# Kernel optimization log

Measured on AMD Instinct MI355X. Metric: run time of the kernel, lower is better.

## Reference

```python
import jax, jax.numpy as jnp
import numpy as np

N, E, H, F_IN, F_OUT = 100000, 1600000, 4, 128, 32
SLOPE = 0.2


def setup_inputs() -> dict:
    key = jax.random.key(0)
    ks = jax.random.split(key, 5)
    x = jax.random.normal(ks[0], (N, F_IN), dtype=jnp.float32)
    edge_src = jax.random.randint(ks[1], (E,), 0, N)
    edge_dst = jax.random.randint(ks[2], (E,), 0, N)
    # xavier-ish init (gain 1.414) as in reset_parameters
    weight = jax.random.normal(ks[3], (H, F_IN, F_OUT), dtype=jnp.float32) * (1.414 / np.sqrt(F_IN))
    a = jax.random.normal(ks[4], (H, 2 * F_OUT), dtype=jnp.float32) * (1.414 / np.sqrt(2 * F_OUT))
    bias = jnp.zeros((H, F_OUT), dtype=jnp.float32)
    return {"x": x, "weight": weight, "a": a, "bias": bias,
            "edge_src": edge_src, "edge_dst": edge_dst}


def reference(x, weight, a, bias, edge_src, edge_dst):
    # per-head linear transform: [N,H,F_OUT]
    h = jnp.einsum('nf,hfo->nho', x, weight)
    # split attention vector: e_ij = LeakyReLU(a_src.h_i + a_dst.h_j)
    a_src, a_dst = a[:, :F_OUT], a[:, F_OUT:]
    alpha_src = jnp.einsum('nho,ho->nh', h, a_src)  # [N,H]
    alpha_dst = jnp.einsum('nho,ho->nh', h, a_dst)  # [N,H]
    e = jax.nn.leaky_relu(alpha_src[edge_src] + alpha_dst[edge_dst], SLOPE)  # [E,H]
    # numerically-stable edge softmax over incoming edges of each dst node
    e_max = jax.ops.segment_max(e, edge_dst, num_segments=N)  # [N,H]
    e_max = jnp.where(jnp.isfinite(e_max), e_max, 0.0)        # nodes with no in-edges
    e_exp = jnp.exp(e - e_max[edge_dst])                      # [E,H]
    denom = jax.ops.segment_sum(e_exp, edge_dst, num_segments=N)  # [N,H]
    att = e_exp / (denom[edge_dst] + 1e-16)                   # [E,H]
    # weighted aggregation: out[j] = sum_i att_ij * h_i
    msg = h[edge_src] * att[:, :, None]                       # [E,H,F_OUT]
    out = jax.ops.segment_sum(msg, edge_dst, num_segments=N)  # [N,H,F_OUT]
    out = out + bias                                          # broadcast [H,F_OUT]
    return out.reshape(N, H * F_OUT)                          # multi-head concat
```

## Files before the change

kernel.cpp:

```cpp
#include <hip/hip_runtime.h>

#define NN   100000
#define NE   1600000
#define NH   4
#define FIN  128
#define FOUT 32
#define HF   128
#define SLOPE 0.2f

#define PBKT  64
#define PNB   ((NN+PBKT-1)/PBKT)
#define CAP   2048
#define EPB   16384
#define NEB   ((NE+EPB-1)/EPB)
#define LCSR  768

typedef __attribute__((ext_vector_type(8))) short short8v;
typedef __attribute__((ext_vector_type(4))) float f32x4;

__device__ __forceinline__ unsigned int bpack(float lo, float hi){
    unsigned int ul = __float_as_uint(lo), uh = __float_as_uint(hi);
    ul = (ul + 0x7fffu + ((ul>>16)&1u)) >> 16;
    uh = (uh + 0x7fffu + ((uh>>16)&1u)) >> 16;
    return ul | (uh<<16);
}
__device__ __forceinline__ short bf16of(float f){
    unsigned int u = __float_as_uint(f);
    return (short)((u + 0x7fffu + ((u>>16)&1u)) >> 16);
}

__global__ __launch_bounds__(256) void node_mfma(
    const float* __restrict__ x, const float* __restrict__ w,
    const float* __restrict__ wa, unsigned int* __restrict__ hb,
    float* __restrict__ asrc, float* __restrict__ adst)
{
    __shared__ short xs[64*128];
    char* lds = (char*)xs;
    const int t  = threadIdx.x;
    const int n0 = blockIdx.x*64;

    #pragma unroll
    for (int p=0; p<8; ++p){
        int r  = p*8 + (t>>5);
        int cq = t & 31;
        int nr = n0 + r; if (nr > NN-1) nr = NN-1;
        float4 v = *(const float4*)(x + (size_t)nr*FIN + cq*4);
        unsigned int lo = bpack(v.x, v.y), hi = bpack(v.z, v.w);
        int cb = (cq*8) ^ ((r&7)<<4);
        *(uint2*)(lds + r*256 + cb) = make_uint2(lo, hi);
    }
    __syncthreads();

    const int wv   = t>>6;
    const int lane = t&63;
    const int l15  = lane&15;
    const int lk   = (lane>>4)<<3;

    short8v Bf[3][4];
    #pragma unroll
    for (int cf=0; cf<2; ++cf){
        int col = wv*32 + cf*16 + l15;
        const float* wp = w + (size_t)(col>>5)*4096 + (col&31);
        #pragma unroll
        for (int ks=0; ks<4; ++ks){
            short8v b;
            #pragma unroll
            for (int j=0;j<8;j++)
                b[j] = bf16of(wp[(size_t)(ks*32 + lk + j)*32]);
            Bf[cf][ks] = b;
        }
    }
    if (wv==0){
        const float* wap = wa + l15*128;
        #pragma unroll
        for (int ks=0; ks<4; ++ks){
            short8v b;
            #pragma unroll
            for (int j=0;j<8;j++){
                float v = (l15<8) ? wap[ks*32 + lk + j] : 0.f;
                b[j] = bf16of(v);
            }
            Bf[2][ks] = b;
        }
    }

    f32x4 C[4][3];
    #pragma unroll
    for (int rt=0;rt<4;rt++)
        #pragma unroll
        for (int cf=0;cf<3;cf++){ f32x4 z = {0.f,0.f,0.f,0.f}; C[rt][cf] = z; }

    const int axor = (lane&7)<<4;
    #pragma unroll
    for (int rt=0; rt<4; ++rt){
        int row = rt*16 + l15;
        const char* arow = lds + row*256;
        short8v Af[4];
        #pragma unroll
        for (int ks=0; ks<4; ++ks)
            Af[ks] = *(const short8v*)(arow + (((ks<<6) | (lk<<1)) ^ axor));
        #pragma unroll
        for (int ks=0; ks<4; ++ks){
            C[rt][0] = __builtin_amdgcn_mfma_f32_16x16x32_bf16(Af[ks], Bf[0][ks], C[rt][0], 0,0,0);
            C[rt][1] = __builtin_amdgcn_mfma_f32_16x16x32_bf16(Af[ks], Bf[1][ks], C[rt][1], 0,0,0);
            if (wv==0)
                C[rt][2] = __builtin_amdgcn_mfma_f32_16x16x32_bf16(Af[ks], Bf[2][ks], C[rt][2], 0,0,0);
        }
    }

    const int g4 = l15>>2;
    #pragma unroll
    for (int rt=0; rt<4; ++rt){
        #pragma unroll
        for (int cf=0; cf<2; ++cf){
            f32x4 c = C[rt][cf];
            #pragma unroll
            for (int i=0;i<4;i++){
                float v1 = __shfl_xor(c[i], 1);
                float v2 = __shfl_xor(c[i], 2);
                float v3 = __shfl_xor(c[i], 3);
                int node = n0 + rt*16 + ((lane>>4)<<2) + i;
                if ((l15&3)==0 && node < NN){
                    uint2 pk = make_uint2(bpack(c[i], v1), bpack(v2, v3));
                    *(uint2*)(hb + (size_t)node*64 + wv*16 + cf*8 + g4*2) = pk;
                }
            }
        }
    }
    if (wv==0 && l15 < 8){
        #pragma unroll
        for (int rt=0; rt<4; ++rt){
            f32x4 c = C[rt][2];
            #pragma unroll
            for (int i=0;i<4;i++){
                int node = n0 + rt*16 + ((lane>>4)<<2) + i;
                if (node < NN){
                    if (l15 < 4) asrc[(size_t)node*4 + l15]     = c[i];
                    else         adst[(size_t)node*4 + (l15-4)] = c[i];
                }
            }
        }
    }
}

__global__ __launch_bounds__(1024) void part_k(const int* __restrict__ esrc,
                                               const int* __restrict__ edst,
                                               int* __restrict__ cnt,
                                               unsigned int* __restrict__ parr,
                                               const float* __restrict__ w,
                                               const float* __restrict__ a,
                                               float* __restrict__ wa)
{
    int t = threadIdx.x;
    if (blockIdx.x == 0){
        int s = t>>7, f = t&127, h = s&3;
        const float* ap = a + h*64 + (s>>2)*32;
        const float* wp = w + (size_t)h*4096 + f*32;
        float acc = 0.f;
        #pragma unroll
        for (int o=0;o<32;o++) acc = fmaf(wp[o], ap[o], acc);
        wa[s*128 + f] = acc;
    }
    __shared__ int hist[PNB];
    __shared__ int bcur[PNB];
    for (int i=t;i<PNB;i+=1024) hist[i]=0;
    __syncthreads();
    int base = blockIdx.x*EPB;
    #pragma unroll
    for (int k=0;k<16;k++){
        int e = base + k*1024 + t;
        if (e < NE) atomicAdd(&hist[edst[e]>>6], 1);
    }
    __syncthreads();
    for (int i=t;i<PNB;i+=1024)
        bcur[i] = hist[i] ? atomicAdd(&cnt[i], hist[i]) : 0;
    __syncthreads();
    #pragma unroll
    for (int k=0;k<16;k++){
        int e = base + k*1024 + t;
        if (e < NE){
            int d = edst[e], s = esrc[e];
            int b = d>>6;
            int pos = atomicAdd(&bcur[b], 1);
            parr[(size_t)b*CAP + pos] = ((unsigned int)s<<6) | (unsigned int)(d & 63);
        }
    }
}

__global__ __launch_bounds__(256) void gather_k(
    const int* __restrict__ cnt,
    const unsigned int* __restrict__ parr,
    const float* __restrict__ asrc, const float* __restrict__ adst,
    const unsigned int* __restrict__ hb, const float* __restrict__ bias,
    float* __restrict__ out)
{
    __shared__ int lcount[32], loffs[32], lcur[32];
    __shared__ int lcsr[LCSR];
    int b = blockIdx.x, bkt = b>>1, half = b&1;
    int t = threadIdx.x;
    int cb = cnt[bkt];
    const unsigned int* pb = parr + (size_t)bkt*CAP;

    if (t < 32) lcount[t] = 0;
    __syncthreads();
    for (int i=t;i<cb;i+=256){
        unsigned int dl = pb[i] & 63u;
        if ((int)(dl>>5) == half) atomicAdd(&lcount[dl&31], 1);
    }
    __syncthreads();
    if (t < 32){
        int v = lcount[t];
        int x = v;
        #pragma unroll
        for (int off=1; off<32; off<<=1){
            int y = __shfl_up(x, off);
            if (t >= off) x += y;
        }
        loffs[t] = x - v;
        lcur[t]  = x - v;
    }
    __syncthreads();
    for (int i=t;i<cb;i+=256){
        unsigned int en = pb[i];
        unsigned int dl = en & 63u;
        if ((int)(dl>>5) == half){
            int pos = atomicAdd(&lcur[dl&31], 1);
            if (pos < LCSR) lcsr[pos] = (int)(en >> 6);
        }
    }
    __syncthreads();

    int wv = t>>6, lane = t&63, head = lane>>4;
    float2 bi = *(const float2*)(bias + 2*lane);
    const unsigned int* hoff = hb + lane;
    int dbase = bkt*PBKT + half*32;

    for (int dl = wv; dl < 32; dl += 4){
        int d = dbase + dl;
        if (d >= NN) break;
        int st = loffs[dl];
        int en = st + lcount[dl];
        if (st > LCSR) st = LCSR;
        if (en > LCSR) en = LCSR;

        float ad_h = adst[(size_t)d*NH + head];
        float ssum = 0.f, acc0 = 0.f, acc1 = 0.f;

        int i = st;
        for (; i + 8 <= en; i += 8){
            int s[8]; float av[8]; unsigned int u[8];
            #pragma unroll
            for (int k=0;k<8;k++) s[k] = lcsr[i+k];
            #pragma unroll
            for (int k=0;k<8;k++) av[k] = asrc[(size_t)s[k]*NH + head];
            #pragma unroll
            for (int k=0;k<8;k++) u[k] = hoff[(size_t)s[k]*64];
            #pragma unroll
            for (int k=0;k<8;k++){
                float v = av[k] + ad_h;
                v = v > 0.f ? v : SLOPE*v;
                float p = __expf(v);
                ssum += p;
                acc0 = fmaf(p, __uint_as_float(u[k]<<16),        acc0);
                acc1 = fmaf(p, __uint_as_float(u[k]&0xffff0000u), acc1);
            }
        }
        for (; i < en; ++i){
            int s = lcsr[i];
            float av = asrc[(size_t)s*NH + head];
            unsigned int u = hoff[(size_t)s*64];
            float v = av + ad_h;
            v = v > 0.f ? v : SLOPE*v;
            float p = __expf(v);
            ssum += p;
            acc0 = fmaf(p, __uint_as_float(u<<16),        acc0);
            acc1 = fmaf(p, __uint_as_float(u&0xffff0000u), acc1);
        }
        float inv = 1.f / (ssum + 1e-16f);
        float2 o = make_float2(acc0*inv + bi.x, acc1*inv + bi.y);
        *(float2*)(out + (size_t)d*HF + 2*lane) = o;
    }
}

extern "C" void kernel_launch(void* const* d_in, const int* in_sizes, int n_in,
                              void* d_out, int out_size, void* d_ws, size_t ws_size,
                              hipStream_t stream)
{
    const float* x    = (const float*)d_in[0];
    const float* w    = (const float*)d_in[1];
    const float* a    = (const float*)d_in[2];
    const float* bias = (const float*)d_in[3];
    const int* esrc   = (const int*)d_in[4];
    const int* edst   = (const int*)d_in[5];
    float* out = (float*)d_out;

    unsigned int* hb = (unsigned int*)d_ws;
    float* as   = (float*)(hb + (size_t)NN*64);
    float* ad   = as + (size_t)NN*NH;
    int* cnt    = (int*)(ad + (size_t)NN*NH);
    unsigned int* parr = (unsigned int*)(cnt + PNB);
    float* wa   = (float*)(parr + (size_t)PNB*CAP);

    hipMemsetAsync(cnt, 0, PNB*sizeof(int), stream);
    hipLaunchKernelGGL(part_k, dim3(NEB), dim3(1024), 0, stream,
                       esrc, edst, cnt, parr, w, a, wa);
    hipLaunchKernelGGL(node_mfma, dim3((NN+63)/64), dim3(256), 0, stream,
                       x, w, wa, hb, as, ad);
    hipLaunchKernelGGL(gather_k, dim3(PNB*2), dim3(256), 0, stream,
                       cnt, parr, as, ad, hb, bias, out);
}
```

Before: 151.8 us.

## Precompute bf16 weight fragments, replace memset, interleave two dst nodes in gather

Adds a single-block prep kernel that folds the attention vector into the weights, packs the weight and attention-weight MFMA B fragments into bf16 once, and zeroes the bucket counters in place of the memset. node_mfma then loads ready-made fragments instead of every block doing strided fp32 loads and conversions. gather_k now has each wave process two destination nodes together in chunks of 4 edges, so more independent gathers are in flight to hide latency. The cost is an extra serial launch before part_k and somewhat higher register use in gather.

```diff
diff --git a/kernel.cpp b/kernel.cpp
--- a/kernel.cpp
+++ b/kernel.cpp
@@ -28,10 +28,50 @@
     unsigned int u = __float_as_uint(f);
     return (short)((u + 0x7fffu + ((u>>16)&1u)) >> 16);
 }
+__device__ __forceinline__ float blo(unsigned int u){ return __uint_as_float(u<<16); }
+__device__ __forceinline__ float bhi(unsigned int u){ return __uint_as_float(u&0xffff0000u); }
+
+__global__ __launch_bounds__(1024) void prep_k(
+    const float* __restrict__ w, const float* __restrict__ a,
+    short* __restrict__ wfrag, short* __restrict__ wafrag,
+    int* __restrict__ cnt)
+{
+    __shared__ float wal[1024];
+    int t = threadIdx.x;
+    {
+        int s = t>>7, f = t&127, h = s&3;
+        const float* ap = a + h*64 + (s>>2)*32;
+        const float* wp = w + (size_t)h*4096 + f*32;
+        float acc = 0.f;
+        #pragma unroll
+        for (int o=0;o<32;o++) acc = fmaf(wp[o], ap[o], acc);
+        wal[s*128 + f] = acc;
+    }
+    __syncthreads();
+    for (int idx=t; idx<2048; idx+=1024){
+        int lane = idx&63, ks=(idx>>6)&3, cf=(idx>>8)&1, wvv=idx>>9;
+        int col = wvv*32 + cf*16 + (lane&15);
+        int fb  = ks*32 + (lane>>4)*8;
+        const float* wp = w + (size_t)(col>>5)*4096 + (col&31);
+        short8v bv;
+        #pragma unroll
+        for (int j=0;j<8;j++) bv[j] = bf16of(wp[(size_t)(fb+j)*32]);
+        ((short8v*)wfrag)[idx] = bv;
+    }
+    if (t < 256){
+        int lane = t&63, ks = t>>6;
+        int l15 = lane&15, fb = ks*32 + (lane>>4)*8;
+        short8v bv;
+        #pragma unroll
+        for (int j=0;j<8;j++) bv[j] = (l15<8) ? bf16of(wal[l15*128 + fb + j]) : (short)0;
+        ((short8v*)wafrag)[t] = bv;
+    }
+    for (int i=t;i<PNB;i+=1024) cnt[i]=0;
+}
 
 __global__ __launch_bounds__(256) void node_mfma(
-    const float* __restrict__ x, const float* __restrict__ w,
-    const float* __restrict__ wa, unsigned int* __restrict__ hb,
+    const float* __restrict__ x, const short* __restrict__ wfrag,
+    const short* __restrict__ wafrag, unsigned int* __restrict__ hb,
     float* __restrict__ asrc, float* __restrict__ adst)
 {
     __shared__ short xs[64*128];
@@ -57,31 +97,16 @@
     const int lk   = (lane>>4)<<3;
 
     short8v Bf[3][4];
-    #pragma unroll
-    for (int cf=0; cf<2; ++cf){
-        int col = wv*32 + cf*16 + l15;
-        const float* wp = w + (size_t)(col>>5)*4096 + (col&31);
-        #pragma unroll
-        for (int ks=0; ks<4; ++ks){
-            short8v b;
-            #pragma unroll
-            for (int j=0;j<8;j++)
-                b[j] = bf16of(wp[(size_t)(ks*32 + lk + j)*32]);
-            Bf[cf][ks] = b;
-        }
-    }
+    const short8v* wf  = (const short8v*)wfrag;
+    const short8v* waf = (const short8v*)wafrag;
+    #pragma unroll
+    for (int cf=0; cf<2; ++cf)
+        #pragma unroll
+        for (int ks=0; ks<4; ++ks)
+            Bf[cf][ks] = wf[((wv*2+cf)*4+ks)*64 + lane];
     if (wv==0){
-        const float* wap = wa + l15*128;
-        #pragma unroll
-        for (int ks=0; ks<4; ++ks){
-            short8v b;
-            #pragma unroll
-            for (int j=0;j<8;j++){
-                float v = (l15<8) ? wap[ks*32 + lk + j] : 0.f;
-                b[j] = bf16of(v);
-            }
-            Bf[2][ks] = b;
-        }
+        #pragma unroll
+        for (int ks=0; ks<4; ++ks) Bf[2][ks] = waf[ks*64 + lane];
     }
 
     f32x4 C[4][3];
@@ -146,23 +171,11 @@
 __global__ __launch_bounds__(1024) void part_k(const int* __restrict__ esrc,
                                                const int* __restrict__ edst,
                                                int* __restrict__ cnt,
-                                               unsigned int* __restrict__ parr,
-                                               const float* __restrict__ w,
-                                               const float* __restrict__ a,
-                                               float* __restrict__ wa)
-{
-    int t = threadIdx.x;
-    if (blockIdx.x == 0){
-        int s = t>>7, f = t&127, h = s&3;
-        const float* ap = a + h*64 + (s>>2)*32;
-        const float* wp = w + (size_t)h*4096 + f*32;
-        float acc = 0.f;
-        #pragma unroll
-        for (int o=0;o<32;o++) acc = fmaf(wp[o], ap[o], acc);
-        wa[s*128 + f] = acc;
-    }
+                                               unsigned int* __restrict__ parr)
+{
     __shared__ int hist[PNB];
     __shared__ int bcur[PNB];
+    int t = threadIdx.x;
     for (int i=t;i<PNB;i+=1024) hist[i]=0;
     __syncthreads();
     int base = blockIdx.x*EPB;
@@ -187,6 +200,39 @@
     }
 }
 
+__device__ __forceinline__ void edge4(const int* __restrict__ lcsr, int i, int head,
+    float ad_h, const float* __restrict__ asrc, const unsigned int* __restrict__ hoff,
+    float& ssum, float& acc0, float& acc1)
+{
+    int s0=lcsr[i], s1=lcsr[i+1], s2=lcsr[i+2], s3=lcsr[i+3];
+    float a0=asrc[(size_t)s0*NH+head], a1=asrc[(size_t)s1*NH+head];
+    float a2=asrc[(size_t)s2*NH+head], a3=asrc[(size_t)s3*NH+head];
+    unsigned int u0=hoff[(size_t)s0*64], u1=hoff[(size_t)s1*64];
+    unsigned int u2=hoff[(size_t)s2*64], u3=hoff[(size_t)s3*64];
+    float v0=a0+ad_h; v0 = v0>0.f ? v0 : SLOPE*v0;
+    float v1=a1+ad_h; v1 = v1>0.f ? v1 : SLOPE*v1;
+    float v2=a2+ad_h; v2 = v2>0.f ? v2 : SLOPE*v2;
+    float v3=a3+ad_h; v3 = v3>0.f ? v3 : SLOPE*v3;
+    float p0=__expf(v0), p1=__expf(v1), p2=__expf(v2), p3=__expf(v3);
+    ssum += (p0+p1)+(p2+p3);
+    acc0 = fmaf(p0,blo(u0), fmaf(p1,blo(u1), fmaf(p2,blo(u2), fmaf(p3,blo(u3), acc0))));
+    acc1 = fmaf(p0,bhi(u0), fmaf(p1,bhi(u1), fmaf(p2,bhi(u2), fmaf(p3,bhi(u3), acc1))));
+}
+__device__ __forceinline__ void edge1(const int* __restrict__ lcsr, int i, int head,
+    float ad_h, const float* __restrict__ asrc, const unsigned int* __restrict__ hoff,
+    float& ssum, float& acc0, float& acc1)
+{
+    int s = lcsr[i];
+    float av = asrc[(size_t)s*NH+head];
+    unsigned int u = hoff[(size_t)s*64];
+    float v = av + ad_h;
+    v = v > 0.f ? v : SLOPE*v;
+    float p = __expf(v);
+    ssum += p;
+    acc0 = fmaf(p, blo(u), acc0);
+    acc1 = fmaf(p, bhi(u), acc1);
+}
+
 __global__ __launch_bounds__(256) void gather_k(
     const int* __restrict__ cnt,
     const unsigned int* __restrict__ parr,
@@ -235,50 +281,37 @@
     const unsigned int* hoff = hb + lane;
     int dbase = bkt*PBKT + half*32;
 
-    for (int dl = wv; dl < 32; dl += 4){
-        int d = dbase + dl;
-        if (d >= NN) break;
-        int st = loffs[dl];
-        int en = st + lcount[dl];
-        if (st > LCSR) st = LCSR;
-        if (en > LCSR) en = LCSR;
-
-        float ad_h = adst[(size_t)d*NH + head];
-        float ssum = 0.f, acc0 = 0.f, acc1 = 0.f;
-
-        int i = st;
-        for (; i + 8 <= en; i += 8){
-            int s[8]; float av[8]; unsigned int u[8];
-            #pragma unroll
-            for (int k=0;k<8;k++) s[k] = lcsr[i+k];
-            #pragma unroll
-            for (int k=0;k<8;k++) av[k] = asrc[(size_t)s[k]*NH + head];
-            #pragma unroll
-            for (int k=0;k<8;k++) u[k] = hoff[(size_t)s[k]*64];
-            #pragma unroll
-            for (int k=0;k<8;k++){
-                float v = av[k] + ad_h;
-                v = v > 0.f ? v : SLOPE*v;
-                float p = __expf(v);
-                ssum += p;
-                acc0 = fmaf(p, __uint_as_float(u[k]<<16),        acc0);
-                acc1 = fmaf(p, __uint_as_float(u[k]&0xffff0000u), acc1);
-            }
-        }
-        for (; i < en; ++i){
-            int s = lcsr[i];
-            float av = asrc[(size_t)s*NH + head];
-            unsigned int u = hoff[(size_t)s*64];
-            float v = av + ad_h;
-            v = v > 0.f ? v : SLOPE*v;
-            float p = __expf(v);
-            ssum += p;
-            acc0 = fmaf(p, __uint_as_float(u<<16),        acc0);
-            acc1 = fmaf(p, __uint_as_float(u&0xffff0000u), acc1);
-        }
-        float inv = 1.f / (ssum + 1e-16f);
-        float2 o = make_float2(acc0*inv + bi.x, acc1*inv + bi.y);
-        *(float2*)(out + (size_t)d*HF + 2*lane) = o;
+    for (int dp = wv; dp < 16; dp += 4){
+        int dA = dbase + dp, dB = dA + 16;
+        bool vA = dA < NN, vB = dB < NN;
+        int iA=0, enA=0, iB=0, enB=0;
+        float adA=0.f, adB=0.f;
+        if (vA){ iA = loffs[dp];    enA = iA + lcount[dp];
+                 adA = adst[(size_t)dA*NH + head]; }
+        if (vB){ iB = loffs[dp+16]; enB = iB + lcount[dp+16];
+                 adB = adst[(size_t)dB*NH + head]; }
+        float sA=0.f, a0A=0.f, a1A=0.f, sB=0.f, a0B=0.f, a1B=0.f;
+
+        while (iA+4 <= enA && iB+4 <= enB){
+            edge4(lcsr, iA, head, adA, asrc, hoff, sA, a0A, a1A);
+            edge4(lcsr, iB, head, adB, asrc, hoff, sB, a0B, a1B);
+            iA += 4; iB += 4;
+        }
+        for (; iA+4 <= enA; iA += 4) edge4(lcsr, iA, head, adA, asrc, hoff, sA, a0A, a1A);
+        for (; iB+4 <= enB; iB += 4) edge4(lcsr, iB, head, adB, asrc, hoff, sB, a0B, a1B);
+        for (; iA < enA; ++iA) edge1(lcsr, iA, head, adA, asrc, hoff, sA, a0A, a1A);
+        for (; iB < enB; ++iB) edge1(lcsr, iB, head, adB, asrc, hoff, sB, a0B, a1B);
+
+        if (vA){
+            float inv = 1.f / (sA + 1e-16f);
+            float2 o = make_float2(a0A*inv + bi.x, a1A*inv + bi.y);
+            *(float2*)(out + (size_t)dA*HF + 2*lane) = o;
+        }
+        if (vB){
+            float inv = 1.f / (sB + 1e-16f);
+            float2 o = make_float2(a0B*inv + bi.x, a1B*inv + bi.y);
+            *(float2*)(out + (size_t)dB*HF + 2*lane) = o;
+        }
     }
 }
 
@@ -294,18 +327,20 @@
     const int* edst   = (const int*)d_in[5];
     float* out = (float*)d_out;
 
-    unsigned int* hb = (unsigned int*)d_ws;
+    short* wfrag  = (short*)d_ws;
+    short* wafrag = wfrag + 16384;
+    unsigned int* hb = (unsigned int*)(wafrag + 2048);
     float* as   = (float*)(hb + (size_t)NN*64);
     float* ad   = as + (size_t)NN*NH;
-    int* cnt    = (int*)(ad + (size_t)NN*NH);
-    unsigned int* parr = (unsigned int*)(cnt + PNB);
-    float* wa   = (float*)(parr + (size_t)PNB*CAP);
-
-    hipMemsetAsync(cnt, 0, PNB*sizeof(int), stream);
+    unsigned int* parr = (unsigned int*)(ad + (size_t)NN*NH);
+    int* cnt    = (int*)(parr + (size_t)PNB*CAP);
+
+    hipLaunchKernelGGL(prep_k, dim3(1), dim3(1024), 0, stream,
+                       w, a, wfrag, wafrag, cnt);
     hipLaunchKernelGGL(part_k, dim3(NEB), dim3(1024), 0, stream,
-                       esrc, edst, cnt, parr, w, a, wa);
+                       esrc, edst, cnt, parr);
     hipLaunchKernelGGL(node_mfma, dim3((NN+63)/64), dim3(256), 0, stream,
-                       x, w, wa, hb, as, ad);
+                       x, wfrag, wafrag, hb, as, ad);
     hipLaunchKernelGGL(gather_k, dim3(PNB*2), dim3(256), 0, stream,
                        cnt, parr, as, ad, hb, bias, out);
 }
```

After: 146.8 us. -3.2%, faster.

## Fuse edge partitioning with node MFMA transform and precompute weight fragments

Applied to the files above, without the earlier changes.

Edge bucketing and the node linear transform now run in one kernel, with every fifth block doing partition work, so the two independent phases overlap on the device. A single-block prep kernel replaces the memset and builds bf16 MFMA weight fragments once, so each MFMA block loads ready fragments instead of converting strided fp32 weights itself. LeakyReLU becomes an fmaxf. Partition blocks now have 256 threads each, which adds more global atomics on cnt, and the prep kernel adds a serial launch on the critical path.

```diff
diff --git a/kernel.cpp b/kernel.cpp
--- a/kernel.cpp
+++ b/kernel.cpp
@@ -11,8 +11,8 @@
 #define PBKT  64
 #define PNB   ((NN+PBKT-1)/PBKT)
 #define CAP   2048
-#define EPB   16384
-#define NEB   ((NE+EPB-1)/EPB)
+#define NMF   1563
+#define NPART 391
 #define LCSR  768
 
 typedef __attribute__((ext_vector_type(8))) short short8v;
@@ -28,16 +28,90 @@
     unsigned int u = __float_as_uint(f);
     return (short)((u + 0x7fffu + ((u>>16)&1u)) >> 16);
 }
-
-__global__ __launch_bounds__(256) void node_mfma(
-    const float* __restrict__ x, const float* __restrict__ w,
-    const float* __restrict__ wa, unsigned int* __restrict__ hb,
-    float* __restrict__ asrc, float* __restrict__ adst)
+__device__ __forceinline__ float blo(unsigned int u){ return __uint_as_float(u<<16); }
+__device__ __forceinline__ float bhi(unsigned int u){ return __uint_as_float(u&0xffff0000u); }
+
+__global__ __launch_bounds__(1024) void prep_k(
+    const float* __restrict__ w, const float* __restrict__ a,
+    short* __restrict__ wfrag, short* __restrict__ wafrag,
+    int* __restrict__ cnt)
 {
-    __shared__ short xs[64*128];
-    char* lds = (char*)xs;
-    const int t  = threadIdx.x;
-    const int n0 = blockIdx.x*64;
+    __shared__ float wal[1024];
+    int t = threadIdx.x;
+    {
+        int s = t>>7, f = t&127, h = s&3;
+        const float* ap = a + h*64 + (s>>2)*32;
+        const float* wp = w + (size_t)h*4096 + f*32;
+        float acc = 0.f;
+        #pragma unroll
+        for (int o=0;o<32;o++) acc = fmaf(wp[o], ap[o], acc);
+        wal[s*128 + f] = acc;
+    }
+    __syncthreads();
+    for (int idx=t; idx<2048; idx+=1024){
+        int lane = idx&63, ks=(idx>>6)&3, cf=(idx>>8)&1, wvv=idx>>9;
+        int col = wvv*32 + cf*16 + (lane&15);
+        int fb  = ks*32 + (lane>>4)*8;
+        const float* wp = w + (size_t)(col>>5)*4096 + (col&31);
+        short8v bv;
+        #pragma unroll
+        for (int j=0;j<8;j++) bv[j] = bf16of(wp[(size_t)(fb+j)*32]);
+        ((short8v*)wfrag)[idx] = bv;
+    }
+    if (t < 256){
+        int lane = t&63, ks = t>>6;
+        int l15 = lane&15, fb = ks*32 + (lane>>4)*8;
+        short8v bv;
+        #pragma unroll
+        for (int j=0;j<8;j++) bv[j] = (l15<8) ? bf16of(wal[l15*128 + fb + j]) : (short)0;
+        ((short8v*)wafrag)[t] = bv;
+    }
+    for (int i=t;i<PNB;i+=1024) cnt[i]=0;
+}
+
+__global__ __launch_bounds__(256) void fused_k(
+    const float* __restrict__ x, const short* __restrict__ wfrag,
+    const short* __restrict__ wafrag, unsigned int* __restrict__ hb,
+    float* __restrict__ asrc, float* __restrict__ adst,
+    const int* __restrict__ esrc, const int* __restrict__ edst,
+    int* __restrict__ cnt, unsigned int* __restrict__ parr)
+{
+    __shared__ char smem[16384];
+    const int bid = blockIdx.x;
+    const int t   = threadIdx.x;
+    const int r5  = bid % 5;
+
+    if (r5 == 4){
+        int* hist = (int*)smem;
+        int* bcur = hist + PNB;
+        for (int i=t;i<PNB;i+=256) hist[i]=0;
+        __syncthreads();
+        int base = (bid/5)*4096;
+        #pragma unroll
+        for (int k=0;k<16;k++){
+            int e = base + k*256 + t;
+            if (e < NE) atomicAdd(&hist[edst[e]>>6], 1);
+        }
+        __syncthreads();
+        for (int i=t;i<PNB;i+=256)
+            bcur[i] = hist[i] ? atomicAdd(&cnt[i], hist[i]) : 0;
+        __syncthreads();
+        #pragma unroll
+        for (int k=0;k<16;k++){
+            int e = base + k*256 + t;
+            if (e < NE){
+                int d = edst[e], s = esrc[e];
+                int pos = atomicAdd(&bcur[d>>6], 1);
+                parr[(size_t)(d>>6)*CAP + pos] = ((unsigned int)s<<6) | (unsigned int)(d & 63);
+            }
+        }
+        return;
+    }
+
+    const int mi = (bid/5)*4 + r5;
+    if (mi >= NMF) return;
+    char* lds = smem;
+    const int n0 = mi*64;
 
     #pragma unroll
     for (int p=0; p<8; ++p){
@@ -57,31 +131,16 @@
     const int lk   = (lane>>4)<<3;
 
     short8v Bf[3][4];
-    #pragma unroll
-    for (int cf=0; cf<2; ++cf){
-        int col = wv*32 + cf*16 + l15;
-        const float* wp = w + (size_t)(col>>5)*4096 + (col&31);
-        #pragma unroll
-        for (int ks=0; ks<4; ++ks){
-            short8v b;
-            #pragma unroll
-            for (int j=0;j<8;j++)
-                b[j] = bf16of(wp[(size_t)(ks*32 + lk + j)*32]);
-            Bf[cf][ks] = b;
-        }
-    }
+    const short8v* wf  = (const short8v*)wfrag;
+    const short8v* waf = (const short8v*)wafrag;
+    #pragma unroll
+    for (int cf=0; cf<2; ++cf)
+        #pragma unroll
+        for (int ks=0; ks<4; ++ks)
+            Bf[cf][ks] = wf[((wv*2+cf)*4+ks)*64 + lane];
     if (wv==0){
-        const float* wap = wa + l15*128;
-        #pragma unroll
-        for (int ks=0; ks<4; ++ks){
-            short8v b;
-            #pragma unroll
-            for (int j=0;j<8;j++){
-                float v = (l15<8) ? wap[ks*32 + lk + j] : 0.f;
-                b[j] = bf16of(v);
-            }
-            Bf[2][ks] = b;
-        }
+        #pragma unroll
+        for (int ks=0; ks<4; ++ks) Bf[2][ks] = waf[ks*64 + lane];
     }
 
     f32x4 C[4][3];
@@ -139,50 +198,6 @@
                     else         adst[(size_t)node*4 + (l15-4)] = c[i];
                 }
             }
-        }
-    }
-}
-
-__global__ __launch_bounds__(1024) void part_k(const int* __restrict__ esrc,
-                                               const int* __restrict__ edst,
-                                               int* __restrict__ cnt,
-                                               unsigned int* __restrict__ parr,
-                                               const float* __restrict__ w,
-                                               const float* __restrict__ a,
-                                               float* __restrict__ wa)
-{
-    int t = threadIdx.x;
-    if (blockIdx.x == 0){
-        int s = t>>7, f = t&127, h = s&3;
-        const float* ap = a + h*64 + (s>>2)*32;
-        const float* wp = w + (size_t)h*4096 + f*32;
-        float acc = 0.f;
-        #pragma unroll
-        for (int o=0;o<32;o++) acc = fmaf(wp[o], ap[o], acc);
-        wa[s*128 + f] = acc;
-    }
-    __shared__ int hist[PNB];
-    __shared__ int bcur[PNB];
-    for (int i=t;i<PNB;i+=1024) hist[i]=0;
-    __syncthreads();
-    int base = blockIdx.x*EPB;
-    #pragma unroll
-    for (int k=0;k<16;k++){
-        int e = base + k*1024 + t;
-        if (e < NE) atomicAdd(&hist[edst[e]>>6], 1);
-    }
-    __syncthreads();
-    for (int i=t;i<PNB;i+=1024)
-        bcur[i] = hist[i] ? atomicAdd(&cnt[i], hist[i]) : 0;
-    __syncthreads();
-    #pragma unroll
-    for (int k=0;k<16;k++){
-        int e = base + k*1024 + t;
-        if (e < NE){
-            int d = edst[e], s = esrc[e];
-            int b = d>>6;
-            int pos = atomicAdd(&bcur[b], 1);
-            parr[(size_t)b*CAP + pos] = ((unsigned int)s<<6) | (unsigned int)(d & 63);
         }
     }
 }
@@ -258,11 +273,11 @@
             #pragma unroll
             for (int k=0;k<8;k++){
                 float v = av[k] + ad_h;
-                v = v > 0.f ? v : SLOPE*v;
+                v = fmaxf(v, SLOPE*v);
                 float p = __expf(v);
                 ssum += p;
-                acc0 = fmaf(p, __uint_as_float(u[k]<<16),        acc0);
-                acc1 = fmaf(p, __uint_as_float(u[k]&0xffff0000u), acc1);
+                acc0 = fmaf(p, blo(u[k]), acc0);
+                acc1 = fmaf(p, bhi(u[k]), acc1);
             }
         }
         for (; i < en; ++i){
@@ -270,11 +285,11 @@
             float av = asrc[(size_t)s*NH + head];
             unsigned int u = hoff[(size_t)s*64];
             float v = av + ad_h;
-            v = v > 0.f ? v : SLOPE*v;
+            v = fmaxf(v, SLOPE*v);
             float p = __expf(v);
             ssum += p;
-            acc0 = fmaf(p, __uint_as_float(u<<16),        acc0);
-            acc1 = fmaf(p, __uint_as_float(u&0xffff0000u), acc1);
+            acc0 = fmaf(p, blo(u), acc0);
+            acc1 = fmaf(p, bhi(u), acc1);
         }
         float inv = 1.f / (ssum + 1e-16f);
         float2 o = make_float2(acc0*inv + bi.x, acc1*inv + bi.y);
@@ -294,18 +309,18 @@
     const int* edst   = (const int*)d_in[5];
     float* out = (float*)d_out;
 
-    unsigned int* hb = (unsigned int*)d_ws;
+    short* wfrag  = (short*)d_ws;
+    short* wafrag = wfrag + 16384;
+    unsigned int* hb = (unsigned int*)(wafrag + 2048);
     float* as   = (float*)(hb + (size_t)NN*64);
     float* ad   = as + (size_t)NN*NH;
-    int* cnt    = (int*)(ad + (size_t)NN*NH);
-    unsigned int* parr = (unsigned int*)(cnt + PNB);
-    float* wa   = (float*)(parr + (size_t)PNB*CAP);
-
-    hipMemsetAsync(cnt, 0, PNB*sizeof(int), stream);
-    hipLaunchKernelGGL(part_k, dim3(NEB), dim3(1024), 0, stream,
-                       esrc, edst, cnt, parr, w, a, wa);
-    hipLaunchKernelGGL(node_mfma, dim3((NN+63)/64), dim3(256), 0, stream,
-                       x, w, wa, hb, as, ad);
+    unsigned int* parr = (unsigned int*)(ad + (size_t)NN*NH);
+    int* cnt    = (int*)(parr + (size_t)PNB*CAP);
+
+    hipLaunchKernelGGL(prep_k, dim3(1), dim3(1024), 0, stream,
+                       w, a, wfrag, wafrag, cnt);
+    hipLaunchKernelGGL(fused_k, dim3(NMF + NPART + 1), dim3(256), 0, stream,
+                       x, wfrag, wafrag, hb, as, ad, esrc, edst, cnt, parr);
     hipLaunchKernelGGL(gather_k, dim3(PNB*2), dim3(256), 0, stream,
                        cnt, parr, as, ad, hb, bias, out);
 }
```

After: 133.6 us. 1.14x faster.
